# Performance work log

Measured on AMD Instinct MI355X. Metric: run time of the kernel, lower is better.

Reference implementation:

```python
import jax, jax.numpy as jnp
import numpy as np

GAMMA = 0.99   # discount_factor
LAM = 0.95     # smoothing_factor

def setup_inputs() -> dict:
    key = jax.random.key(0)
    k1, k2, k3, k4 = jax.random.split(key, 4)
    B, T = 4096, 2048
    return {
        "rewards": jax.random.normal(k1, (B, T), dtype=jnp.float32),
        "values": jax.random.normal(k2, (B, T), dtype=jnp.float32),
        "next_value": jax.random.normal(k3, (B,), dtype=jnp.float32),
        "done_flags": jax.random.randint(k4, (B, T), 0, 2, dtype=jnp.int32),
    }

def reference(rewards, values, next_value, done_flags):
    d = done_flags.astype(rewards.dtype)
    # next_non_terminal[t] = 1 - done[t+1] for t < T-1, and 1 - done[T-1] at t = T-1
    nnt = 1.0 - jnp.concatenate([d[..., 1:], d[..., -1:]], axis=-1)
    # next value at step t: values[t+1] for t < T-1, bootstrap next_value at t = T-1
    nv = jnp.concatenate([values[..., 1:], next_value[..., None]], axis=-1)
    delta = rewards + GAMMA * nv * nnt - values  # [B, T]

    def step(gae, x):
        dl, nn = x
        gae = dl + GAMMA * LAM * nn * gae
        return gae, gae

    # scan backward over time (leading axis for lax.scan)
    deltaT = jnp.moveaxis(delta, -1, 0)  # [T, B]
    nntT = jnp.moveaxis(nnt, -1, 0)      # [T, B]
    init = jnp.zeros(rewards.shape[:-1], rewards.dtype)
    _, advT = jax.lax.scan(step, init, (deltaT, nntT), reverse=True)
    advantages = jnp.moveaxis(advT, 0, -1)  # [B, T]
    returns = advantages + values
    return advantages, returns
```

## Files before the change

### kernel.cpp

```cpp
#include <hip/hip_runtime.h>

#define GAMMA 0.99f
#define LAM   0.95f

constexpr int BLOCK = 256;
constexpr int CHUNK = 8;
constexpr int NWAVES = BLOCK / 64;

__global__ __launch_bounds__(BLOCK) void gae_scan_kernel(
    const float* __restrict__ rewards,
    const float* __restrict__ values,
    const float* __restrict__ next_value,
    const int*   __restrict__ done,
    float* __restrict__ adv_out,
    float* __restrict__ ret_out,
    int T)
{
    const int row  = blockIdx.x;
    const int tid  = threadIdx.x;
    const int lane = tid & 63;
    const int wave = tid >> 6;

    const long rowbase = (long)row * T;
    const int  col0    = tid * CHUNK;

    float r[CHUNK], v[CHUNK];
    const float4* r4 = reinterpret_cast<const float4*>(rewards + rowbase + col0);
    const float4* v4 = reinterpret_cast<const float4*>(values  + rowbase + col0);
    float4 ra = r4[0], rb = r4[1];
    float4 va = v4[0], vb = v4[1];
    r[0]=ra.x; r[1]=ra.y; r[2]=ra.z; r[3]=ra.w;
    r[4]=rb.x; r[5]=rb.y; r[6]=rb.z; r[7]=rb.w;
    v[0]=va.x; v[1]=va.y; v[2]=va.z; v[3]=va.w;
    v[4]=vb.x; v[5]=vb.y; v[6]=vb.z; v[7]=vb.w;

    const float vnext_last = (col0 + CHUNK < T) ? values[rowbase + col0 + CHUNK]
                                                : next_value[row];

    float delta[CHUNK], c[CHUNK];
#pragma unroll
    for (int j = 0; j < CHUNK; ++j) {
        const int tcol = col0 + j;
        const int dcol = (tcol + 1 < T) ? (tcol + 1) : (T - 1);
        const float nnt = 1.0f - (float)done[rowbase + dcol];
        const float nv  = (j < CHUNK - 1) ? v[j + 1] : vnext_last;
        delta[j] = r[j] + GAMMA * nv * nnt - v[j];
        c[j]     = (GAMMA * LAM) * nnt;
    }

    float a = 0.0f, m = 1.0f;
#pragma unroll
    for (int j = CHUNK - 1; j >= 0; --j) {
        a = delta[j] + c[j] * a;
        m = c[j] * m;
    }

    float sa = a, sm = m;
#pragma unroll
    for (int d = 1; d < 64; d <<= 1) {
        float oa = __shfl_down(sa, d);
        float om = __shfl_down(sm, d);
        if (lane + d < 64) { sa = sa + sm * oa; sm = sm * om; }
    }
    float ea = __shfl_down(sa, 1);
    float em = __shfl_down(sm, 1);
    if (lane == 63) { ea = 0.0f; em = 1.0f; }

    __shared__ float lds_a[NWAVES];
    __shared__ float lds_m[NWAVES];
    if (lane == 0) { lds_a[wave] = sa; lds_m[wave] = sm; }
    __syncthreads();

    float g = 0.0f;
    for (int j = NWAVES - 1; j > wave; --j)
        g = lds_a[j] + lds_m[j] * g;
    float gin = ea + em * g;

    float adv[CHUNK];
#pragma unroll
    for (int j = CHUNK - 1; j >= 0; --j) {
        gin = delta[j] + c[j] * gin;
        adv[j] = gin;
    }

    float4* a4 = reinterpret_cast<float4*>(adv_out + rowbase + col0);
    float4* t4 = reinterpret_cast<float4*>(ret_out + rowbase + col0);
    a4[0] = make_float4(adv[0], adv[1], adv[2], adv[3]);
    a4[1] = make_float4(adv[4], adv[5], adv[6], adv[7]);
    t4[0] = make_float4(adv[0] + v[0], adv[1] + v[1], adv[2] + v[2], adv[3] + v[3]);
    t4[1] = make_float4(adv[4] + v[4], adv[5] + v[5], adv[6] + v[6], adv[7] + v[7]);
}

__global__ void gae_naive_kernel(
    const float* __restrict__ rewards,
    const float* __restrict__ values,
    const float* __restrict__ next_value,
    const int*   __restrict__ done,
    float* __restrict__ adv_out,
    float* __restrict__ ret_out,
    int B, int T)
{
    int row = blockIdx.x * blockDim.x + threadIdx.x;
    if (row >= B) return;
    long base = (long)row * T;
    float g = 0.0f;
    for (int t = T - 1; t >= 0; --t) {
        int dcol = (t + 1 < T) ? (t + 1) : (T - 1);
        float nnt = 1.0f - (float)done[base + dcol];
        float nv  = (t + 1 < T) ? values[base + t + 1] : next_value[row];
        float dl  = rewards[base + t] + GAMMA * nv * nnt - values[base + t];
        g = dl + (GAMMA * LAM) * nnt * g;
        adv_out[base + t] = g;
        ret_out[base + t] = g + values[base + t];
    }
}

extern "C" void kernel_launch(void* const* d_in, const int* in_sizes, int n_in,
                              void* d_out, int out_size, void* d_ws, size_t ws_size,
                              hipStream_t stream) {
    const float* rewards    = (const float*)d_in[0];
    const float* values     = (const float*)d_in[1];
    const float* next_value = (const float*)d_in[2];
    const int*   done       = (const int*)d_in[3];

    const int B = in_sizes[2];
    const int T = in_sizes[0] / B;

    float* adv = (float*)d_out;
    float* ret = adv + (long)B * T;

    if (T == BLOCK * CHUNK) {
        gae_scan_kernel<<<B, BLOCK, 0, stream>>>(
            rewards, values, next_value, done, adv, ret, T);
    } else {
        gae_naive_kernel<<<(B + 255) / 256, 256, 0, stream>>>(
            rewards, values, next_value, done, adv, ret, B, T);
    }
}
```

Baseline: 147.9 us.

## Use persistent blocks with next-row prefetch and vectorized done loads

Switches the scan kernel to a persistent grid of up to 1024 blocks, each looping over rows and prefetching the next row's rewards, values and done flags into registers while the current row is computed. The per-element scalar done loads are replaced with int4 vector loads, and neighbour values and flags now come from lane shuffles plus a single boundary load. The LDS partials are double-buffered by parity so the next row's writes do not race with the current row's reads. This aims to hide global-memory latency and cut load instructions, at the cost of more registers per thread and fewer blocks in flight.

```diff
diff --git a/kernel.cpp b/kernel.cpp
--- a/kernel.cpp
+++ b/kernel.cpp
@@ -3,92 +3,137 @@
 #define GAMMA 0.99f
 #define LAM   0.95f
 
-constexpr int BLOCK = 256;
-constexpr int CHUNK = 8;
+constexpr int BLOCK  = 256;
+constexpr int CHUNK  = 8;
 constexpr int NWAVES = BLOCK / 64;
+constexpr int GRID_TARGET = 1024;
 
-__global__ __launch_bounds__(BLOCK) void gae_scan_kernel(
+typedef float f32x4 __attribute__((ext_vector_type(4)));
+
+struct RowRegs {
+    float4 ra, rb, va, vb;
+    int4   da, db;
+    float  bv;
+    int    bd;
+    float  vboot;
+};
+
+__device__ __forceinline__ void load_row(
+    const float* __restrict__ rewards, const float* __restrict__ values,
+    const float* __restrict__ next_value, const int* __restrict__ done,
+    int row, int T, int col0, int lane, int tid, RowRegs& R)
+{
+    const long rowbase = (long)row * T;
+    const float4* r4 = reinterpret_cast<const float4*>(rewards + rowbase + col0);
+    const float4* v4 = reinterpret_cast<const float4*>(values  + rowbase + col0);
+    const int4*   d4 = reinterpret_cast<const int4*>(done      + rowbase + col0);
+    R.ra = r4[0]; R.rb = r4[1];
+    R.va = v4[0]; R.vb = v4[1];
+    R.da = d4[0]; R.db = d4[1];
+    if (lane == 63) {
+        const int bcol = (col0 + CHUNK < T) ? (col0 + CHUNK) : (T - 1);
+        R.bv = values[rowbase + bcol];
+        R.bd = done[rowbase + bcol];
+    }
+    if (tid == BLOCK - 1) R.vboot = next_value[row];
+}
+
+__global__ __launch_bounds__(BLOCK, 4) void gae_scan_kernel(
     const float* __restrict__ rewards,
     const float* __restrict__ values,
     const float* __restrict__ next_value,
     const int*   __restrict__ done,
     float* __restrict__ adv_out,
     float* __restrict__ ret_out,
-    int T)
+    int B, int T)
 {
-    const int row  = blockIdx.x;
     const int tid  = threadIdx.x;
     const int lane = tid & 63;
     const int wave = tid >> 6;
+    const int col0 = tid * CHUNK;
 
-    const long rowbase = (long)row * T;
-    const int  col0    = tid * CHUNK;
+    __shared__ float lds_a[2][NWAVES];
+    __shared__ float lds_m[2][NWAVES];
 
-    float r[CHUNK], v[CHUNK];
-    const float4* r4 = reinterpret_cast<const float4*>(rewards + rowbase + col0);
-    const float4* v4 = reinterpret_cast<const float4*>(values  + rowbase + col0);
-    float4 ra = r4[0], rb = r4[1];
-    float4 va = v4[0], vb = v4[1];
-    r[0]=ra.x; r[1]=ra.y; r[2]=ra.z; r[3]=ra.w;
-    r[4]=rb.x; r[5]=rb.y; r[6]=rb.z; r[7]=rb.w;
-    v[0]=va.x; v[1]=va.y; v[2]=va.z; v[3]=va.w;
-    v[4]=vb.x; v[5]=vb.y; v[6]=vb.z; v[7]=vb.w;
+    RowRegs cur, nxt;
+    load_row(rewards, values, next_value, done, blockIdx.x, T, col0, lane, tid, cur);
 
-    const float vnext_last = (col0 + CHUNK < T) ? values[rowbase + col0 + CHUNK]
-                                                : next_value[row];
+    int parity = 0;
+    for (int row = blockIdx.x; row < B; row += gridDim.x) {
+        const int nrow = row + gridDim.x;
+        if (nrow < B)
+            load_row(rewards, values, next_value, done, nrow, T, col0, lane, tid, nxt);
 
-    float delta[CHUNK], c[CHUNK];
+        const long rowbase = (long)row * T;
+
+        float v[CHUNK], r[CHUNK];
+        v[0]=cur.va.x; v[1]=cur.va.y; v[2]=cur.va.z; v[3]=cur.va.w;
+        v[4]=cur.vb.x; v[5]=cur.vb.y; v[6]=cur.vb.z; v[7]=cur.vb.w;
+        r[0]=cur.ra.x; r[1]=cur.ra.y; r[2]=cur.ra.z; r[3]=cur.ra.w;
+        r[4]=cur.rb.x; r[5]=cur.rb.y; r[6]=cur.rb.z; r[7]=cur.rb.w;
+
+        const float v_nb = __shfl_down(cur.va.x, 1);
+        const int   d_nb = __shfl_down(cur.da.x, 1);
+        float vnext  = (lane == 63) ? cur.bv : v_nb;
+        float dnextf = (float)((lane == 63) ? cur.bd : d_nb);
+        if (tid == BLOCK - 1) vnext = cur.vboot;
+
+        float dn[CHUNK];
+        dn[0]=(float)cur.da.y; dn[1]=(float)cur.da.z; dn[2]=(float)cur.da.w; dn[3]=(float)cur.db.x;
+        dn[4]=(float)cur.db.y; dn[5]=(float)cur.db.z; dn[6]=(float)cur.db.w; dn[7]=dnextf;
+        float nv[CHUNK];
+        nv[0]=v[1]; nv[1]=v[2]; nv[2]=v[3]; nv[3]=v[4];
+        nv[4]=v[5]; nv[5]=v[6]; nv[6]=v[7]; nv[7]=vnext;
+
+        float delta[CHUNK], c[CHUNK];
 #pragma unroll
-    for (int j = 0; j < CHUNK; ++j) {
-        const int tcol = col0 + j;
-        const int dcol = (tcol + 1 < T) ? (tcol + 1) : (T - 1);
-        const float nnt = 1.0f - (float)done[rowbase + dcol];
-        const float nv  = (j < CHUNK - 1) ? v[j + 1] : vnext_last;
-        delta[j] = r[j] + GAMMA * nv * nnt - v[j];
-        c[j]     = (GAMMA * LAM) * nnt;
+        for (int j = 0; j < CHUNK; ++j) {
+            const float nnt = 1.0f - dn[j];
+            delta[j] = r[j] + GAMMA * nv[j] * nnt - v[j];
+            c[j]     = (GAMMA * LAM) * nnt;
+        }
+
+        float a = 0.0f, m = 1.0f;
+#pragma unroll
+        for (int j = CHUNK - 1; j >= 0; --j) {
+            a = delta[j] + c[j] * a;
+            m = c[j] * m;
+        }
+
+        float sa = a, sm = m;
+#pragma unroll
+        for (int d = 1; d < 64; d <<= 1) {
+            float oa = __shfl_down(sa, d);
+            float om = __shfl_down(sm, d);
+            if (lane + d < 64) { sa = sa + sm * oa; sm = sm * om; }
+        }
+        float ea = __shfl_down(sa, 1);
+        float em = __shfl_down(sm, 1);
+        if (lane == 63) { ea = 0.0f; em = 1.0f; }
+
+        if (lane == 0) { lds_a[parity][wave] = sa; lds_m[parity][wave] = sm; }
+        __syncthreads();
+        float g = 0.0f;
+        for (int j = NWAVES - 1; j > wave; --j)
+            g = lds_a[parity][j] + lds_m[parity][j] * g;
+        float gin = ea + em * g;
+
+#pragma unroll
+        for (int j = CHUNK - 1; j >= 0; --j) {
+            gin = delta[j] + c[j] * gin;
+            delta[j] = gin;
+        }
+
+        float4* a4 = reinterpret_cast<float4*>(adv_out + rowbase + col0);
+        float4* t4 = reinterpret_cast<float4*>(ret_out + rowbase + col0);
+        a4[0] = make_float4(delta[0], delta[1], delta[2], delta[3]);
+        a4[1] = make_float4(delta[4], delta[5], delta[6], delta[7]);
+        t4[0] = make_float4(delta[0]+v[0], delta[1]+v[1], delta[2]+v[2], delta[3]+v[3]);
+        t4[1] = make_float4(delta[4]+v[4], delta[5]+v[5], delta[6]+v[6], delta[7]+v[7]);
+
+        parity ^= 1;
+        cur = nxt;
     }
-
-    float a = 0.0f, m = 1.0f;
-#pragma unroll
-    for (int j = CHUNK - 1; j >= 0; --j) {
-        a = delta[j] + c[j] * a;
-        m = c[j] * m;
-    }
-
-    float sa = a, sm = m;
-#pragma unroll
-    for (int d = 1; d < 64; d <<= 1) {
-        float oa = __shfl_down(sa, d);
-        float om = __shfl_down(sm, d);
-        if (lane + d < 64) { sa = sa + sm * oa; sm = sm * om; }
-    }
-    float ea = __shfl_down(sa, 1);
-    float em = __shfl_down(sm, 1);
-    if (lane == 63) { ea = 0.0f; em = 1.0f; }
-
-    __shared__ float lds_a[NWAVES];
-    __shared__ float lds_m[NWAVES];
-    if (lane == 0) { lds_a[wave] = sa; lds_m[wave] = sm; }
-    __syncthreads();
-
-    float g = 0.0f;
-    for (int j = NWAVES - 1; j > wave; --j)
-        g = lds_a[j] + lds_m[j] * g;
-    float gin = ea + em * g;
-
-    float adv[CHUNK];
-#pragma unroll
-    for (int j = CHUNK - 1; j >= 0; --j) {
-        gin = delta[j] + c[j] * gin;
-        adv[j] = gin;
-    }
-
-    float4* a4 = reinterpret_cast<float4*>(adv_out + rowbase + col0);
-    float4* t4 = reinterpret_cast<float4*>(ret_out + rowbase + col0);
-    a4[0] = make_float4(adv[0], adv[1], adv[2], adv[3]);
-    a4[1] = make_float4(adv[4], adv[5], adv[6], adv[7]);
-    t4[0] = make_float4(adv[0] + v[0], adv[1] + v[1], adv[2] + v[2], adv[3] + v[3]);
-    t4[1] = make_float4(adv[4] + v[4], adv[5] + v[5], adv[6] + v[6], adv[7] + v[7]);
 }
 
 __global__ void gae_naive_kernel(
@@ -130,8 +175,9 @@
     float* ret = adv + (long)B * T;
 
     if (T == BLOCK * CHUNK) {
-        gae_scan_kernel<<<B, BLOCK, 0, stream>>>(
-            rewards, values, next_value, done, adv, ret, T);
+        const int grid = (B < GRID_TARGET) ? B : GRID_TARGET;
+        gae_scan_kernel<<<grid, BLOCK, 0, stream>>>(
+            rewards, values, next_value, done, adv, ret, B, T);
     } else {
         gae_naive_kernel<<<(B + 255) / 256, 256, 0, stream>>>(
             rewards, values, next_value, done, adv, ret, B, T);
```

After: 150.6 us. About the same (+1.8%).

## Map one row per wavefront with 32-element chunks, dropping cross-wave LDS combine

Applied to the files above, without the earlier changes.

Each row is now handled by a single 64-lane wavefront, with each lane owning 32 contiguous timesteps, instead of a 256-thread block per row. This removes the shared-memory partial exchange and the __syncthreads between waves. Done flags are now loaded with vectorized int4 reads, and the neighbour value and flag come from a lane shuffle rather than scalar global loads. The trade-off is much higher register pressure from 32-element arrays per lane, which may reduce occupancy. Lane memory accesses are also strided by 128 bytes, which may hurt coalescing.

```diff
diff --git a/kernel.cpp b/kernel.cpp
--- a/kernel.cpp
+++ b/kernel.cpp
@@ -3,47 +3,61 @@
 #define GAMMA 0.99f
 #define LAM   0.95f
 
-constexpr int BLOCK = 256;
-constexpr int CHUNK = 8;
-constexpr int NWAVES = BLOCK / 64;
+constexpr int CHUNK = 32;
+constexpr int WPB   = 4;
+constexpr int BLOCK = WPB * 64;
 
-__global__ __launch_bounds__(BLOCK) void gae_scan_kernel(
+__global__ __launch_bounds__(BLOCK) void gae_wave_kernel(
     const float* __restrict__ rewards,
     const float* __restrict__ values,
     const float* __restrict__ next_value,
     const int*   __restrict__ done,
     float* __restrict__ adv_out,
     float* __restrict__ ret_out,
-    int T)
+    int B, int T)
 {
-    const int row  = blockIdx.x;
-    const int tid  = threadIdx.x;
-    const int lane = tid & 63;
-    const int wave = tid >> 6;
+    const int wave = threadIdx.x >> 6;
+    const int lane = threadIdx.x & 63;
+    const int row  = blockIdx.x * WPB + wave;
+    if (row >= B) return;
 
     const long rowbase = (long)row * T;
-    const int  col0    = tid * CHUNK;
+    const int  col0    = lane * CHUNK;
 
-    float r[CHUNK], v[CHUNK];
     const float4* r4 = reinterpret_cast<const float4*>(rewards + rowbase + col0);
     const float4* v4 = reinterpret_cast<const float4*>(values  + rowbase + col0);
-    float4 ra = r4[0], rb = r4[1];
-    float4 va = v4[0], vb = v4[1];
-    r[0]=ra.x; r[1]=ra.y; r[2]=ra.z; r[3]=ra.w;
-    r[4]=rb.x; r[5]=rb.y; r[6]=rb.z; r[7]=rb.w;
-    v[0]=va.x; v[1]=va.y; v[2]=va.z; v[3]=va.w;
-    v[4]=vb.x; v[5]=vb.y; v[6]=vb.z; v[7]=vb.w;
+    const int4*   d4 = reinterpret_cast<const int4*>(done      + rowbase + col0);
 
-    const float vnext_last = (col0 + CHUNK < T) ? values[rowbase + col0 + CHUNK]
-                                                : next_value[row];
+    float4 ra[8], va[8];
+    int4   da[8];
+#pragma unroll
+    for (int k = 0; k < 8; ++k) { ra[k] = r4[k]; }
+#pragma unroll
+    for (int k = 0; k < 8; ++k) { va[k] = v4[k]; }
+#pragma unroll
+    for (int k = 0; k < 8; ++k) { da[k] = d4[k]; }
+    const float vboot = next_value[row];
+
+    float v[CHUNK], r[CHUNK];
+    int   d[CHUNK];
+#pragma unroll
+    for (int k = 0; k < 8; ++k) {
+        v[4*k+0]=va[k].x; v[4*k+1]=va[k].y; v[4*k+2]=va[k].z; v[4*k+3]=va[k].w;
+        r[4*k+0]=ra[k].x; r[4*k+1]=ra[k].y; r[4*k+2]=ra[k].z; r[4*k+3]=ra[k].w;
+        d[4*k+0]=da[k].x; d[4*k+1]=da[k].y; d[4*k+2]=da[k].z; d[4*k+3]=da[k].w;
+    }
+
+    const float v_nb = __shfl_down(v[0], 1);
+    const int   d_nb = __shfl_down(d[0], 1);
+    const float vnext  = (lane == 63) ? vboot : v_nb;
+    const int   dnext  = (lane == 63) ? d[CHUNK-1] : d_nb;
 
     float delta[CHUNK], c[CHUNK];
 #pragma unroll
     for (int j = 0; j < CHUNK; ++j) {
-        const int tcol = col0 + j;
-        const int dcol = (tcol + 1 < T) ? (tcol + 1) : (T - 1);
-        const float nnt = 1.0f - (float)done[rowbase + dcol];
-        const float nv  = (j < CHUNK - 1) ? v[j + 1] : vnext_last;
+        const int   dn  = (j < CHUNK-1) ? d[j+1] : dnext;
+        const float nv  = (j < CHUNK-1) ? v[j+1] : vnext;
+        const float nnt = 1.0f - (float)dn;
         delta[j] = r[j] + GAMMA * nv * nnt - v[j];
         c[j]     = (GAMMA * LAM) * nnt;
     }
@@ -57,38 +71,29 @@
 
     float sa = a, sm = m;
 #pragma unroll
-    for (int d = 1; d < 64; d <<= 1) {
-        float oa = __shfl_down(sa, d);
-        float om = __shfl_down(sm, d);
-        if (lane + d < 64) { sa = sa + sm * oa; sm = sm * om; }
+    for (int dd = 1; dd < 64; dd <<= 1) {
+        float oa = __shfl_down(sa, dd);
+        float om = __shfl_down(sm, dd);
+        if (lane + dd < 64) { sa = sa + sm * oa; sm = sm * om; }
     }
-    float ea = __shfl_down(sa, 1);
-    float em = __shfl_down(sm, 1);
-    if (lane == 63) { ea = 0.0f; em = 1.0f; }
+    float gin = __shfl_down(sa, 1);
+    if (lane == 63) gin = 0.0f;
 
-    __shared__ float lds_a[NWAVES];
-    __shared__ float lds_m[NWAVES];
-    if (lane == 0) { lds_a[wave] = sa; lds_m[wave] = sm; }
-    __syncthreads();
-
-    float g = 0.0f;
-    for (int j = NWAVES - 1; j > wave; --j)
-        g = lds_a[j] + lds_m[j] * g;
-    float gin = ea + em * g;
-
-    float adv[CHUNK];
 #pragma unroll
     for (int j = CHUNK - 1; j >= 0; --j) {
         gin = delta[j] + c[j] * gin;
-        adv[j] = gin;
+        delta[j] = gin;
     }
 
     float4* a4 = reinterpret_cast<float4*>(adv_out + rowbase + col0);
     float4* t4 = reinterpret_cast<float4*>(ret_out + rowbase + col0);
-    a4[0] = make_float4(adv[0], adv[1], adv[2], adv[3]);
-    a4[1] = make_float4(adv[4], adv[5], adv[6], adv[7]);
-    t4[0] = make_float4(adv[0] + v[0], adv[1] + v[1], adv[2] + v[2], adv[3] + v[3]);
-    t4[1] = make_float4(adv[4] + v[4], adv[5] + v[5], adv[6] + v[6], adv[7] + v[7]);
+#pragma unroll
+    for (int k = 0; k < 8; ++k)
+        a4[k] = make_float4(delta[4*k+0], delta[4*k+1], delta[4*k+2], delta[4*k+3]);
+#pragma unroll
+    for (int k = 0; k < 8; ++k)
+        t4[k] = make_float4(delta[4*k+0]+v[4*k+0], delta[4*k+1]+v[4*k+1],
+                            delta[4*k+2]+v[4*k+2], delta[4*k+3]+v[4*k+3]);
 }
 
 __global__ void gae_naive_kernel(
@@ -129,9 +134,10 @@
     float* adv = (float*)d_out;
     float* ret = adv + (long)B * T;
 
-    if (T == BLOCK * CHUNK) {
-        gae_scan_kernel<<<B, BLOCK, 0, stream>>>(
-            rewards, values, next_value, done, adv, ret, T);
+    if (T == 64 * CHUNK) {
+        const int grid = (B + WPB - 1) / WPB;
+        gae_wave_kernel<<<grid, BLOCK, 0, stream>>>(
+            rewards, values, next_value, done, adv, ret, B, T);
     } else {
         gae_naive_kernel<<<(B + 255) / 256, 256, 0, stream>>>(
             rewards, values, next_value, done, adv, ret, B, T);
```

New measurement: 158.1 us. +6.9%, slower.

## Split GAE scan into per-wave segment summary and apply kernels

Applied to the files above, without the earlier changes.

Replaces the one-block-per-row scan with two kernels: each wave scans a 256-element segment and writes a (sum, multiplier) summary to workspace, then a second pass recomputes the deltas, combines the summaries of later segments serially and writes the outputs. Loads become fully vectorized float4/int4 per lane with neighbor values fetched by shuffle, and block-level synchronization is removed. The cost is reading all inputs twice and adding a second launch plus a small workspace.

```diff
diff --git a/kernel.cpp b/kernel.cpp
--- a/kernel.cpp
+++ b/kernel.cpp
@@ -3,92 +3,131 @@
 #define GAMMA 0.99f
 #define LAM   0.95f
 
-constexpr int BLOCK = 256;
-constexpr int CHUNK = 8;
-constexpr int NWAVES = BLOCK / 64;
+constexpr int SEG   = 256;
+constexpr int WPB   = 4;
+constexpr int BLOCK = WPB * 64;
 
-__global__ __launch_bounds__(BLOCK) void gae_scan_kernel(
-    const float* __restrict__ rewards,
-    const float* __restrict__ values,
-    const float* __restrict__ next_value,
-    const int*   __restrict__ done,
-    float* __restrict__ adv_out,
-    float* __restrict__ ret_out,
-    int T)
+
+__device__ __forceinline__ void seg_delta_c(
+    const float* __restrict__ rewards, const float* __restrict__ values,
+    const float* __restrict__ next_value, const int* __restrict__ done,
+    int row, int seg, int lane, int T,
+    float delta[4], float c[4], float4& vv_out)
 {
-    const int row  = blockIdx.x;
-    const int tid  = threadIdx.x;
-    const int lane = tid & 63;
-    const int wave = tid >> 6;
+    const long rowbase = (long)row * T;
+    const int  col0    = seg * SEG + lane * 4;
 
-    const long rowbase = (long)row * T;
-    const int  col0    = tid * CHUNK;
+    const float4 rv = *reinterpret_cast<const float4*>(rewards + rowbase + col0);
+    const float4 vv = *reinterpret_cast<const float4*>(values  + rowbase + col0);
+    const int4   dv = *reinterpret_cast<const int4*>(done      + rowbase + col0);
 
-    float r[CHUNK], v[CHUNK];
-    const float4* r4 = reinterpret_cast<const float4*>(rewards + rowbase + col0);
-    const float4* v4 = reinterpret_cast<const float4*>(values  + rowbase + col0);
-    float4 ra = r4[0], rb = r4[1];
-    float4 va = v4[0], vb = v4[1];
-    r[0]=ra.x; r[1]=ra.y; r[2]=ra.z; r[3]=ra.w;
-    r[4]=rb.x; r[5]=rb.y; r[6]=rb.z; r[7]=rb.w;
-    v[0]=va.x; v[1]=va.y; v[2]=va.z; v[3]=va.w;
-    v[4]=vb.x; v[5]=vb.y; v[6]=vb.z; v[7]=vb.w;
+    float bv = 0.0f; float bd = 0.0f;
+    if (lane == 63) {
+        const int E = seg * SEG + SEG;
+        if (E < T) { bv = values[rowbase + E]; bd = (float)done[rowbase + E]; }
+        else       { bv = next_value[row];     bd = (float)dv.w; }
+    }
+    const float v_nb = __shfl_down(vv.x, 1);
+    const float d_nb = (float)__shfl_down(dv.x, 1);
+    const float vnext = (lane == 63) ? bv : v_nb;
+    const float dnext = (lane == 63) ? bd : d_nb;
 
-    const float vnext_last = (col0 + CHUNK < T) ? values[rowbase + col0 + CHUNK]
-                                                : next_value[row];
+    const float n0 = 1.0f - (float)dv.y;
+    const float n1 = 1.0f - (float)dv.z;
+    const float n2 = 1.0f - (float)dv.w;
+    const float n3 = 1.0f - dnext;
+    delta[0] = rv.x + GAMMA * vv.y  * n0 - vv.x;
+    delta[1] = rv.y + GAMMA * vv.z  * n1 - vv.y;
+    delta[2] = rv.z + GAMMA * vv.w  * n2 - vv.z;
+    delta[3] = rv.w + GAMMA * vnext * n3 - vv.w;
+    c[0] = (GAMMA * LAM) * n0;
+    c[1] = (GAMMA * LAM) * n1;
+    c[2] = (GAMMA * LAM) * n2;
+    c[3] = (GAMMA * LAM) * n3;
+    vv_out = vv;
+}
 
-    float delta[CHUNK], c[CHUNK];
-#pragma unroll
-    for (int j = 0; j < CHUNK; ++j) {
-        const int tcol = col0 + j;
-        const int dcol = (tcol + 1 < T) ? (tcol + 1) : (T - 1);
-        const float nnt = 1.0f - (float)done[rowbase + dcol];
-        const float nv  = (j < CHUNK - 1) ? v[j + 1] : vnext_last;
-        delta[j] = r[j] + GAMMA * nv * nnt - v[j];
-        c[j]     = (GAMMA * LAM) * nnt;
-    }
-
-    float a = 0.0f, m = 1.0f;
-#pragma unroll
-    for (int j = CHUNK - 1; j >= 0; --j) {
-        a = delta[j] + c[j] * a;
-        m = c[j] * m;
-    }
-
-    float sa = a, sm = m;
+__device__ __forceinline__ void suffix_scan(int lane, float& sa, float& sm)
+{
 #pragma unroll
     for (int d = 1; d < 64; d <<= 1) {
         float oa = __shfl_down(sa, d);
         float om = __shfl_down(sm, d);
         if (lane + d < 64) { sa = sa + sm * oa; sm = sm * om; }
     }
+}
+
+__global__ __launch_bounds__(BLOCK) void gae_sum_kernel(
+    const float* __restrict__ rewards, const float* __restrict__ values,
+    const float* __restrict__ next_value, const int* __restrict__ done,
+    float2* __restrict__ summ,
+    int B, int T)
+{
+    const int S    = T / SEG;
+    const int gw   = blockIdx.x * WPB + (threadIdx.x >> 6);
+    const int lane = threadIdx.x & 63;
+    if (gw >= B * S) return;
+    const int row = gw / S, seg = gw % S;
+
+    float delta[4], c[4]; float4 vv;
+    seg_delta_c(rewards, values, next_value, done, row, seg, lane, T, delta, c, vv);
+
+    float a = 0.0f, m = 1.0f;
+#pragma unroll
+    for (int j = 3; j >= 0; --j) { a = delta[j] + c[j] * a; m = c[j] * m; }
+
+    float sa = a, sm = m;
+    suffix_scan(lane, sa, sm);
+    if (lane == 0) summ[(long)row * S + seg] = make_float2(sa, sm);
+}
+
+__global__ __launch_bounds__(BLOCK) void gae_apply_kernel(
+    const float* __restrict__ rewards, const float* __restrict__ values,
+    const float* __restrict__ next_value, const int* __restrict__ done,
+    const float2* __restrict__ summ,
+    float* __restrict__ adv_out, float* __restrict__ ret_out,
+    int B, int T)
+{
+    const int S    = T / SEG;
+    const int gw   = blockIdx.x * WPB + (threadIdx.x >> 6);
+    const int lane = threadIdx.x & 63;
+    if (gw >= B * S) return;
+    const int row = gw / S, seg = gw % S;
+
+    float delta[4], c[4]; float4 vv;
+    seg_delta_c(rewards, values, next_value, done, row, seg, lane, T, delta, c, vv);
+
+    float a = 0.0f, m = 1.0f;
+#pragma unroll
+    for (int j = 3; j >= 0; --j) { a = delta[j] + c[j] * a; m = c[j] * m; }
+
+    float sa = a, sm = m;
+    suffix_scan(lane, sa, sm);
     float ea = __shfl_down(sa, 1);
     float em = __shfl_down(sm, 1);
     if (lane == 63) { ea = 0.0f; em = 1.0f; }
 
-    __shared__ float lds_a[NWAVES];
-    __shared__ float lds_m[NWAVES];
-    if (lane == 0) { lds_a[wave] = sa; lds_m[wave] = sm; }
-    __syncthreads();
-
     float g = 0.0f;
-    for (int j = NWAVES - 1; j > wave; --j)
-        g = lds_a[j] + lds_m[j] * g;
+    const float2* rs = summ + (long)row * S;
+    for (int j = S - 1; j > seg; --j) {
+        const float2 s = rs[j];
+        g = s.x + s.y * g;
+    }
     float gin = ea + em * g;
 
-    float adv[CHUNK];
 #pragma unroll
-    for (int j = CHUNK - 1; j >= 0; --j) {
+    for (int j = 3; j >= 0; --j) {
         gin = delta[j] + c[j] * gin;
-        adv[j] = gin;
+        delta[j] = gin;
     }
 
+    const long rowbase = (long)row * T;
+    const int  col0    = seg * SEG + lane * 4;
     float4* a4 = reinterpret_cast<float4*>(adv_out + rowbase + col0);
     float4* t4 = reinterpret_cast<float4*>(ret_out + rowbase + col0);
-    a4[0] = make_float4(adv[0], adv[1], adv[2], adv[3]);
-    a4[1] = make_float4(adv[4], adv[5], adv[6], adv[7]);
-    t4[0] = make_float4(adv[0] + v[0], adv[1] + v[1], adv[2] + v[2], adv[3] + v[3]);
-    t4[1] = make_float4(adv[4] + v[4], adv[5] + v[5], adv[6] + v[6], adv[7] + v[7]);
+    *a4 = make_float4(delta[0], delta[1], delta[2], delta[3]);
+    *t4 = make_float4(delta[0] + vv.x, delta[1] + vv.y,
+                      delta[2] + vv.z, delta[3] + vv.w);
 }
 
 __global__ void gae_naive_kernel(
@@ -129,9 +168,16 @@
     float* adv = (float*)d_out;
     float* ret = adv + (long)B * T;
 
-    if (T == BLOCK * CHUNK) {
-        gae_scan_kernel<<<B, BLOCK, 0, stream>>>(
-            rewards, values, next_value, done, adv, ret, T);
+    const long   nseg     = (T % SEG == 0) ? (long)B * (T / SEG) : 0;
+    const size_t ws_need  = (size_t)nseg * sizeof(float2);
+
+    if (nseg > 0 && ws_size >= ws_need) {
+        float2* summ = (float2*)d_ws;
+        const int blocks = (int)((nseg + WPB - 1) / WPB);
+        gae_sum_kernel<<<blocks, BLOCK, 0, stream>>>(
+            rewards, values, next_value, done, summ, B, T);
+        gae_apply_kernel<<<blocks, BLOCK, 0, stream>>>(
+            rewards, values, next_value, done, summ, adv, ret, B, T);
     } else {
         gae_naive_kernel<<<(B + 255) / 256, 256, 0, stream>>>(
             rewards, values, next_value, done, adv, ret, B, T);
```

New measurement: 160.5 us. 8.5% more time.
